# Kernel tuning notes

Hardware: AMD Instinct MI355X
Metric: run time of the kernel (lower is better)

Reference implementation:

```python
import jax, jax.numpy as jnp
import numpy as np

# torch mode -> jnp.pad mode: reflect->'reflect', replicate->'edge', circular->'wrap'
# Input layout: [N, C, H, W]. torch 4-tuple pads act on (W, H); 6-tuple pads act on (W, H, C).

def setup_inputs() -> dict:
    key = jax.random.key(0)
    x = jax.random.normal(key, (16, 32, 512, 512), dtype=jnp.float32)
    return {"x": x}


def _pad_chain(x):
    # 1) F.pad(x, (1,1,0,0), 'reflect')      -> W +-1
    x = jnp.pad(x, ((0, 0), (0, 0), (0, 0), (1, 1)), mode="reflect")
    # 2) F.pad(x, (0,0,2,2), 'reflect')      -> H +-2
    x = jnp.pad(x, ((0, 0), (0, 0), (2, 2), (0, 0)), mode="reflect")
    # 3) F.pad(x, (0,0,2,2), 'replicate')    -> H +-2 (edge)
    x = jnp.pad(x, ((0, 0), (0, 0), (2, 2), (0, 0)), mode="edge")
    # 4) F.pad(x, (0,0,0,0,1,1), 'circular') -> C +-1 (wrap)
    x = jnp.pad(x, ((0, 0), (1, 1), (0, 0), (0, 0)), mode="wrap")
    # 5) F.pad(x, (0,0,0,0,3,3), 'circular') -> C +-3 (wrap)
    x = jnp.pad(x, ((0, 0), (3, 3), (0, 0), (0, 0)), mode="wrap")
    # 6) F.pad(x, (1,1,3,0,0,3), 'replicate')-> W +-1, H +3 front, C +3 back
    x = jnp.pad(x, ((0, 0), (0, 3), (3, 0), (1, 1)), mode="edge")
    # 7) F.pad(x, (1,1,3,0,0,3), 'reflect')  -> W +-1, H +3 front, C +3 back
    x = jnp.pad(x, ((0, 0), (0, 3), (3, 0), (1, 1)), mode="reflect")
    return x


def reference(x) -> jnp.ndarray:
    return _pad_chain(x)
```

## Files before the change

kernel.cpp:

```cpp
#include <hip/hip_runtime.h>


using f4 = __attribute__((ext_vector_type(4))) float;

__device__ __forceinline__ int hmap(int d) {
    if (d <= 8)   return 2;
    if (d == 9)   return 1;
    if (d <= 521) return d - 10;
    return (d == 522) ? 510 : 509;
}

__device__ __forceinline__ int cmap(int g) {
    if (g >= 43) g = 84 - g;
    if (g > 39)  g = 39;
    int p = g - 3;
    if (p < 0)   p += 34;
    if (p >= 34) p -= 34;
    return (p == 0) ? 31 : ((p <= 32) ? (p - 1) : 0);
}

__device__ __forceinline__ const float* in_row_ptr(const float* __restrict__ x,
                                                   unsigned int row) {
    const unsigned int nc = row / 526u;
    const int h  = (int)(row - nc * 526u);
    const int c  = (int)(nc % 46u);
    const int n  = (int)(nc / 46u);
    return x + ((((size_t)n * 32 + cmap(c)) * 512 + hmap(h)) << 9);
}

__global__ __launch_bounds__(256) void pad_rows_kernel(const float* __restrict__ x,
                                                       float* __restrict__ out) {
    const int tt   = threadIdx.x & 127;
    const int half = threadIdx.x >> 7;
    const unsigned int base = blockIdx.x * 4u;
    const unsigned int rowA = base + half;
    const unsigned int rowB = rowA + 2u;

    const float* inA = in_row_ptr(x, rowA);
    const float* inB = in_row_ptr(x, rowB);
    float* outA = out + (size_t)rowA * 518;
    float* outB = out + (size_t)rowB * 518;

    const f4 a = reinterpret_cast<const f4*>(inA)[tt];
    const f4 b = reinterpret_cast<const f4*>(inB)[tt];

    *reinterpret_cast<f4*>(outA + 3 + 4 * tt) = a;
    *reinterpret_cast<f4*>(outB + 3 + 4 * tt) = b;

    if (tt == 0) {
        const float ea = a.y, eb = b.y;
        outA[0] = ea; outA[1] = ea; outA[2] = ea;
        outB[0] = eb; outB[1] = eb; outB[2] = eb;
    } else if (tt == 127) {
        const float ea = a.z, eb = b.z;
        outA[515] = ea; outA[516] = ea; outA[517] = ea;
        outB[515] = eb; outB[516] = eb; outB[517] = eb;
    }
}

extern "C" void kernel_launch(void* const* d_in, const int* in_sizes, int n_in,
                              void* d_out, int out_size, void* d_ws, size_t ws_size,
                              hipStream_t stream) {
    const float* x = (const float*)d_in[0];
    float* out = (float*)d_out;
    pad_rows_kernel<<<96784, 256, 0, stream>>>(x, out);
}
```

Before: 273.0 us.

## Reorder output channel rows so duplicate input reads hit cache together

Output channel slices are processed in a permuted order from a lookup table, so output channels that read the same input channel are grouped next to each other. Block IDs are also swizzled across the 8 XCDs (d&7 times a stride), so each XCD handles a contiguous logical range. The goal is to turn repeated input reads into L2/MALL hits and cut HBM read traffic. The cost is extra index arithmetic and output writes that are no longer in sequential order.

```diff
diff --git a/kernel.cpp b/kernel.cpp
--- a/kernel.cpp
+++ b/kernel.cpp
@@ -2,6 +2,15 @@
 
 
 using f4 = __attribute__((ext_vector_type(4))) float;
+
+__device__ const unsigned char cperm_tab[46] = {
+    2, 4, 36, 38,
+    5, 39, 40, 41, 42, 43, 44, 45,
+    6, 7, 8, 9, 10, 11, 12, 13, 14, 15, 16, 17, 18, 19,
+    20, 21, 22, 23, 24, 25, 26, 27, 28, 29, 30, 31, 32, 33,
+    0, 34,
+    1, 3, 35, 37
+};
 
 __device__ __forceinline__ int hmap(int d) {
     if (d <= 8)   return 2;
@@ -10,36 +19,40 @@
     return (d == 522) ? 510 : 509;
 }
 
-__device__ __forceinline__ int cmap(int g) {
-    if (g >= 43) g = 84 - g;
-    if (g > 39)  g = 39;
-    int p = g - 3;
-    if (p < 0)   p += 34;
-    if (p >= 34) p -= 34;
-    return (p == 0) ? 31 : ((p <= 32) ? (p - 1) : 0);
-}
-
-__device__ __forceinline__ const float* in_row_ptr(const float* __restrict__ x,
-                                                   unsigned int row) {
-    const unsigned int nc = row / 526u;
-    const int h  = (int)(row - nc * 526u);
-    const int c  = (int)(nc % 46u);
-    const int n  = (int)(nc / 46u);
-    return x + ((((size_t)n * 32 + cmap(c)) * 512 + hmap(h)) << 9);
+__device__ __forceinline__ void row_ptrs(const float* __restrict__ x,
+                                         float* __restrict__ out,
+                                         unsigned int lrow,
+                                         const float** pin, float** pout) {
+    const unsigned int p  = lrow / 526u;
+    const int          h  = (int)(lrow - p * 526u);
+    const unsigned int n  = p / 46u;
+    const unsigned int po = p - n * 46u;
+    const int c = cperm_tab[po];
+    int ci;
+    if      (po < 4)  ci = 0;
+    else if (po < 12) ci = 1;
+    else if (po < 40) ci = (int)po - 10;
+    else if (po < 42) ci = 30;
+    else              ci = 31;
+    *pin  = x   + ((((size_t)n * 32 + ci) * 512 + hmap(h)) << 9);
+    *pout = out + ((size_t)(n * 46u + (unsigned)c) * 526u + (unsigned)h) * 518u;
 }
 
 __global__ __launch_bounds__(256) void pad_rows_kernel(const float* __restrict__ x,
                                                        float* __restrict__ out) {
+    const unsigned int d = blockIdx.x;
+    const unsigned int l = (d & 7u) * 12098u + (d >> 3);
+
     const int tt   = threadIdx.x & 127;
     const int half = threadIdx.x >> 7;
-    const unsigned int base = blockIdx.x * 4u;
-    const unsigned int rowA = base + half;
-    const unsigned int rowB = rowA + 2u;
+    const unsigned int base  = l * 4u;
+    const unsigned int lrowA = base + half;
+    const unsigned int lrowB = lrowA + 2u;
 
-    const float* inA = in_row_ptr(x, rowA);
-    const float* inB = in_row_ptr(x, rowB);
-    float* outA = out + (size_t)rowA * 518;
-    float* outB = out + (size_t)rowB * 518;
+    const float *inA, *inB;
+    float *outA, *outB;
+    row_ptrs(x, out, lrowA, &inA, &outA);
+    row_ptrs(x, out, lrowB, &inB, &outB);
 
     const f4 a = reinterpret_cast<const f4*>(inA)[tt];
     const f4 b = reinterpret_cast<const f4*>(inB)[tt];
```

Result: faster. 248.5 us, median of 2 (-9.0%).
